# Performance work log

Measured on AMD Instinct MI355X. Metric: run time of the kernel, lower is better.

The kernel has to match this reference:

```python
import jax, jax.numpy as jnp
import numpy as np

B, S, D, H = 2, 2048, 1024, 16
HD = D // H  # head_dim = 64
ROPE_BASE = 10000.0


def setup_inputs() -> dict:
    key = jax.random.key(0)
    ks = jax.random.split(key, 5)
    scale = 1.0 / np.sqrt(D)
    return {
        "x": jax.random.normal(ks[0], (B, S, D), dtype=jnp.float32),
        "Wq": jax.random.normal(ks[1], (D, D), dtype=jnp.float32) * scale,
        "Wk": jax.random.normal(ks[2], (D, D), dtype=jnp.float32) * scale,
        "Wv": jax.random.normal(ks[3], (D, D), dtype=jnp.float32) * scale,
        "Wo": jax.random.normal(ks[4], (D, D), dtype=jnp.float32) * scale,
    }


def _rotate_half(x):
    x1, x2 = x[..., : HD // 2], x[..., HD // 2:]
    return jnp.concatenate((-x2, x1), axis=-1)


def _rope_cos_sin(seq_len):
    inv_freq = 1.0 / (ROPE_BASE ** (jnp.arange(0, HD, 2, dtype=jnp.float32) / HD))
    t = jnp.arange(seq_len, dtype=jnp.float32)
    freqs = jnp.outer(t, inv_freq)          # [S, HD/2]
    emb = jnp.concatenate((freqs, freqs), -1)  # [S, HD]
    return jnp.cos(emb), jnp.sin(emb)


def reference(x, Wq, Wk, Wv, Wo):
    # projections (torch Linear: y = x @ W.T), split heads -> [B, H, S, HD]
    def proj(W):
        return (x @ W.T).reshape(B, S, H, HD).transpose(0, 2, 1, 3)

    q, k, v = proj(Wq), proj(Wk), proj(Wv)

    cos, sin = _rope_cos_sin(S)  # [S, HD] each, broadcast over B, H
    q = q * cos + _rotate_half(q) * sin
    k = k * cos + _rotate_half(k) * sin

    scale = 1.0 / np.sqrt(HD)
    scores = jnp.einsum("bhsd,bhtd->bhst", q, k) * scale  # [B,H,S,S]
    attn = jax.nn.softmax(scores, axis=-1)
    out = jnp.einsum("bhst,bhtd->bhsd", attn, v)           # [B,H,S,HD]
    out = out.transpose(0, 2, 1, 3).reshape(B, S, D)
    return out @ Wo.T
```

## Files before the change

### kernel.cpp

```cpp
#include <hip/hip_runtime.h>
#include <hip/hip_bf16.h>
#include <math.h>
#include <stdint.h>

typedef __bf16 bf16;
typedef __bf16 bf16x8 __attribute__((ext_vector_type(8)));
typedef __bf16 bf16x4 __attribute__((ext_vector_type(4)));
typedef float  f32x4  __attribute__((ext_vector_type(4)));

#define MFMA16(a,b,c) __builtin_amdgcn_mfma_f32_16x16x32_bf16((a),(b),(c),0,0,0)
#define GLOAD_LDS16(g, l) \
  __builtin_amdgcn_global_load_lds((__attribute__((address_space(1))) void*)(g), \
                                   (__attribute__((address_space(3))) void*)(l), 16, 0, 0)

static constexpr int kB  = 2;
static constexpr int kS  = 2048;
static constexpr int kD  = 1024;
static constexpr int kH  = 16;
static constexpr int kHD = 64;
static constexpr int kM  = kB * kS;
static constexpr float kExpC = 0.125f * 1.44269504f;

__global__ void cvt_all(const float* __restrict__ x,
                        const float* __restrict__ wq, const float* __restrict__ wk,
                        const float* __restrict__ wv, const float* __restrict__ wo,
                        bf16* __restrict__ xb,
                        bf16* __restrict__ wqb, bf16* __restrict__ wkb,
                        bf16* __restrict__ wvb, bf16* __restrict__ wob,
                        float2* __restrict__ rtab)
{
  const int i = blockIdx.x * 256 + threadIdx.x;
  const int NX4 = (kM * kD) / 4;
  const int NW4 = (kD * kD) / 4;
  if (i >= NX4 + 4 * NW4) {
    const int idx = i - (NX4 + 4 * NW4);
    const int s = idx >> 5, d = idx & 31;
    const float f = exp2f(-(float)d * 0.4152410118609203f);
    float sn, cs;
    sincosf((float)s * f, &sn, &cs);
    rtab[idx] = make_float2(cs, sn);
    return;
  }
  const float* src; bf16* dst; int off;
  if (i < NX4) { src = x; dst = xb; off = i; }
  else {
    const int j = i - NX4;
    const int seg = j >> 18;
    off = j & (NW4 - 1);
    src = (seg == 0) ? wq : (seg == 1) ? wk : (seg == 2) ? wv : wo;
    dst = (seg == 0) ? wqb : (seg == 1) ? wkb : (seg == 2) ? wvb : wob;
  }
  const float4 v = ((const float4*)src)[off];
  bf16x4 o = { (bf16)v.x, (bf16)v.y, (bf16)v.z, (bf16)v.w };
  ((bf16x4*)dst)[off] = o;
}

__device__ __forceinline__ void gemm_core_128(
    const bf16* __restrict__ A, const bf16* __restrict__ Bw,
    int m0, int n0, int K, bf16* aT, bf16* bT, f32x4 acc[4][4])
{
  const int t = threadIdx.x, lane = t & 63, wave = t >> 6;
  const int wm = wave >> 1, wn = wave & 1;
  const int srow = lane >> 2;
  const int scol = (lane & 3) * 8;
  for (int k0 = 0; k0 < K; k0 += 32) {
    __syncthreads();
#pragma unroll
    for (int c = 0; c < 2; ++c) {
      const int row = c * 64 + wave * 16 + srow;
      const bf16* ga = A  + (size_t)(m0 + row) * K + k0 + scol;
      const bf16* gb = Bw + (size_t)(n0 + row) * K + k0 + scol;
      GLOAD_LDS16(ga, aT + c * 2048 + wave * 512);
      GLOAD_LDS16(gb, bT + c * 2048 + wave * 512);
    }
    __syncthreads();
    bf16x8 af[4], bfr[4];
#pragma unroll
    for (int i = 0; i < 4; ++i) {
      af[i]  = *(const bf16x8*)(aT + (wm * 64 + i * 16 + (lane & 15)) * 32 + (lane >> 4) * 8);
      bfr[i] = *(const bf16x8*)(bT + (wn * 64 + i * 16 + (lane & 15)) * 32 + (lane >> 4) * 8);
    }
#pragma unroll
    for (int i = 0; i < 4; ++i)
#pragma unroll
      for (int j = 0; j < 4; ++j)
        acc[i][j] = MFMA16(af[i], bfr[j], acc[i][j]);
  }
}

__global__ __launch_bounds__(256) void proj_qkv(
    const bf16* __restrict__ xb,
    const bf16* __restrict__ wqb, const bf16* __restrict__ wkb, const bf16* __restrict__ wvb,
    bf16* __restrict__ Qb, bf16* __restrict__ Kb, bf16* __restrict__ Vt,
    const float2* __restrict__ rtab)
{
  __shared__ __align__(16) bf16 aT[4096];
  __shared__ __align__(16) bf16 bT[4096];
  __shared__ __align__(16) bf16 vtr[2 * 64 * 136];
  const int z = blockIdx.z;
  const bf16* Ww = (z == 0) ? wqb : (z == 1) ? wkb : wvb;
  const int m0 = blockIdx.x * 128, n0 = blockIdx.y * 128;
  f32x4 acc[4][4] = {};
  gemm_core_128(xb, Ww, m0, n0, kD, aT, bT, acc);

  const int lane = threadIdx.x & 63, wave = threadIdx.x >> 6;
  const int wm = wave >> 1, wn = wave & 1, quad = lane >> 4, lc = lane & 15;
  const int hh = (n0 >> 6) + wn;
  if (z == 2) {
#pragma unroll
    for (int i = 0; i < 4; ++i)
#pragma unroll
      for (int j = 0; j < 4; ++j) {
        bf16x4 p;
#pragma unroll
        for (int r = 0; r < 4; ++r) p[r] = (bf16)acc[i][j][r];
        *(bf16x4*)&vtr[(wn * 64 + j * 16 + lc) * 136 + wm * 64 + i * 16 + quad * 4] = p;
      }
    __syncthreads();
    const int t = threadIdx.x;
    const int row = t >> 1;
    const int sh = (t & 1) * 64;
    const int bidx = m0 >> 11;
    const int hh2 = (n0 >> 6) + (row >> 6);
    const int d = row & 63;
    bf16* dst = Vt + ((size_t)(bidx * kH + hh2) * kHD + d) * kS + (m0 & 2047) + sh;
#pragma unroll
    for (int u = 0; u < 8; ++u)
      *(uint4*)(dst + u * 8) = *(const uint4*)&vtr[row * 136 + sh + u * 8];
  } else {
    bf16* Op = (z == 0) ? Qb : Kb;
    const float f = (z == 0) ? kExpC : 1.0f;
#pragma unroll
    for (int j = 0; j < 2; ++j) {
      const int d = j * 16 + lc;
#pragma unroll
      for (int i = 0; i < 4; ++i)
#pragma unroll
        for (int r = 0; r < 4; ++r) {
          const int m = m0 + wm * 64 + i * 16 + quad * 4 + r;
          const int bidx = m >> 11, s = m & 2047;
          const float2 cs = rtab[s * 32 + d];
          const float v0 = acc[i][j][r], v1 = acc[i][j + 2][r];
          bf16* dst = Op + ((size_t)(bidx * kH + hh) * kS + s) * kHD;
          dst[d]      = (bf16)((v0 * cs.x - v1 * cs.y) * f);
          dst[d + 32] = (bf16)((v1 * cs.x + v0 * cs.y) * f);
        }
    }
  }
}

__global__ __launch_bounds__(256, 2) void attn(
    const bf16* __restrict__ Qb, const bf16* __restrict__ Kb,
    const bf16* __restrict__ Vt, bf16* __restrict__ Ob)
{
  __shared__ __align__(16) bf16 kT[128 * 72];
  __shared__ __align__(16) bf16 vT[64 * 136];
  const int t = threadIdx.x, lane = t & 63, wave = t >> 6;
  const int quad = lane >> 4, lc = lane & 15;
  const int bid = blockIdx.x;
  const int qt = (bid >> 3) & 15;
  const int bh = (bid & 7) * 4 + (bid >> 7);
  const size_t base = (size_t)bh * kS * kHD;
  const bf16* Qp = Qb + base + (size_t)qt * 128 * kHD;
  const bf16* Kp = Kb + base;
  const bf16* Vp = Vt + base;

  bf16x8 qf[2][2];
#pragma unroll
  for (int tm = 0; tm < 2; ++tm)
#pragma unroll
    for (int ks = 0; ks < 2; ++ks)
      qf[tm][ks] = *(const bf16x8*)(Qp + (wave * 32 + tm * 16 + lc) * kHD + ks * 32 + quad * 8);

  f32x4 oacc[2][4] = {};
  f32x4 lacc[2] = {};
  const bf16 one = (bf16)1.0f;
  const bf16x8 ones = { one, one, one, one, one, one, one, one };

  const int srow = t >> 1, shalf = (t & 1) * 32;
  const int vd = t >> 2, vc = t & 3;

  for (int kt = 0; kt < kS / 128; ++kt) {
    __syncthreads();
    {
      const bf16* ksrc = Kp + (size_t)(kt * 128 + srow) * kHD + shalf;
#pragma unroll
      for (int u = 0; u < 4; ++u)
        *(uint4*)&kT[srow * 72 + shalf + u * 8] = *(const uint4*)(ksrc + u * 8);
      const bf16* vsrc = Vp + (size_t)vd * kS + kt * 128 + vc * 32;
#pragma unroll
      for (int u = 0; u < 4; ++u)
        *(uint4*)&vT[vd * 136 + vc * 32 + u * 8] = *(const uint4*)(vsrc + u * 8);
    }
    __syncthreads();

    bf16x8 kf[8][2];
#pragma unroll
    for (int nk = 0; nk < 8; ++nk)
#pragma unroll
      for (int ks = 0; ks < 2; ++ks)
        kf[nk][ks] = *(const bf16x8*)&kT[(nk * 16 + lc) * 72 + ks * 32 + quad * 8];

    bf16x8 pfrag[2][4];
#pragma unroll
    for (int tm = 0; tm < 2; ++tm) {
      f32x4 sc[8] = {};
#pragma unroll
      for (int nk = 0; nk < 8; ++nk) {
        sc[nk] = MFMA16(kf[nk][0], qf[tm][0], sc[nk]);
        sc[nk] = MFMA16(kf[nk][1], qf[tm][1], sc[nk]);
      }
#pragma unroll
      for (int kp = 0; kp < 4; ++kp) {
        bf16x8 p;
#pragma unroll
        for (int j = 0; j < 4; ++j) {
          p[j]     = (bf16)__builtin_amdgcn_exp2f(sc[2 * kp][j]);
          p[j + 4] = (bf16)__builtin_amdgcn_exp2f(sc[2 * kp + 1][j]);
        }
        pfrag[tm][kp] = p;
      }
    }

#pragma unroll
    for (int kp = 0; kp < 4; ++kp)
#pragma unroll
      for (int tm = 0; tm < 2; ++tm)
        lacc[tm] = MFMA16(pfrag[tm][kp], ones, lacc[tm]);

#pragma unroll
    for (int nd = 0; nd < 4; ++nd)
#pragma unroll
      for (int kp = 0; kp < 4; ++kp) {
        const bf16x4 lo = *(const bf16x4*)&vT[(nd * 16 + lc) * 136 + kp * 32 + quad * 4];
        const bf16x4 hi = *(const bf16x4*)&vT[(nd * 16 + lc) * 136 + kp * 32 + 16 + quad * 4];
        const bf16x8 vfr = __builtin_shufflevector(lo, hi, 0, 1, 2, 3, 4, 5, 6, 7);
#pragma unroll
        for (int tm = 0; tm < 2; ++tm)
          oacc[tm][nd] = MFMA16(pfrag[tm][kp], vfr, oacc[tm][nd]);
      }
  }

  const int b = bh >> 4, h = bh & 15;
#pragma unroll
  for (int tm = 0; tm < 2; ++tm)
#pragma unroll
    for (int r = 0; r < 4; ++r) {
      const float inv = 1.0f / lacc[tm][r];
      const int s = qt * 128 + wave * 32 + tm * 16 + quad * 4 + r;
      bf16* dst = Ob + ((size_t)(b * kS + s)) * kD + h * kHD;
#pragma unroll
      for (int nd = 0; nd < 4; ++nd)
        dst[nd * 16 + lc] = (bf16)(oacc[tm][nd][r] * inv);
    }
}

__global__ __launch_bounds__(256) void out_proj(
    const bf16* __restrict__ Ab, const bf16* __restrict__ wob, float* __restrict__ Cout)
{
  __shared__ __align__(16) bf16 aT[4096];
  __shared__ __align__(16) bf16 bT[4096];
  const int m0 = blockIdx.x * 128, n0 = blockIdx.y * 128;
  f32x4 acc[4][4] = {};
  gemm_core_128(Ab, wob, m0, n0, kD, aT, bT, acc);
  const int lane = threadIdx.x & 63, wave = threadIdx.x >> 6;
  const int wm = wave >> 1, wn = wave & 1, quad = lane >> 4, lc = lane & 15;
#pragma unroll
  for (int i = 0; i < 4; ++i)
#pragma unroll
    for (int r = 0; r < 4; ++r) {
      const int m = m0 + wm * 64 + i * 16 + quad * 4 + r;
#pragma unroll
      for (int j = 0; j < 4; ++j)
        Cout[(size_t)m * kD + n0 + wn * 64 + j * 16 + lc] = acc[i][j][r];
    }
}

extern "C" void kernel_launch(void* const* d_in, const int* in_sizes, int n_in,
                              void* d_out, int out_size, void* d_ws, size_t ws_size,
                              hipStream_t stream)
{
  const float* x  = (const float*)d_in[0];
  const float* wq = (const float*)d_in[1];
  const float* wk = (const float*)d_in[2];
  const float* wv = (const float*)d_in[3];
  const float* wo = (const float*)d_in[4];
  float* out = (float*)d_out;

  char* ws = (char*)d_ws;
  const size_t MB = 1024 * 1024;
  if (ws_size < 57 * MB) return;
  bf16* xb  = (bf16*)(ws + 0 * MB);
  bf16* wqb = (bf16*)(ws + 8 * MB);
  bf16* wkb = (bf16*)(ws + 10 * MB);
  bf16* wvb = (bf16*)(ws + 12 * MB);
  bf16* wob = (bf16*)(ws + 14 * MB);
  bf16* Qb  = (bf16*)(ws + 16 * MB);
  bf16* Kb  = (bf16*)(ws + 24 * MB);
  bf16* Ob  = (bf16*)(ws + 40 * MB);
  float2* rtab = (float2*)(ws + 48 * MB);
  bf16* Vtp = (bf16*)(ws + 49 * MB);

  cvt_all<<<8448, 256, 0, stream>>>(x, wq, wk, wv, wo, xb, wqb, wkb, wvb, wob, rtab);
  proj_qkv<<<dim3(32, 8, 3), 256, 0, stream>>>(xb, wqb, wkb, wvb, Qb, Kb, Vtp, rtab);
  attn<<<dim3(512), 256, 0, stream>>>(Qb, Kb, Vtp, Ob);
  out_proj<<<dim3(32, 8), 256, 0, stream>>>(Ob, wob, out);
}
```

Baseline: 194.0 us.

## Register-prefetch next tiles in GEMM and attention loops to overlap loads

Both the shared GEMM core and the attention kernel now load the next K-step or KV tile from global memory into registers before computing on the current tile. That data is written to LDS at the start of the next iteration. The GEMM drops the direct global-to-LDS load path in favour of a register-staged double buffer. The aim is to hide global memory latency behind the MFMA work, at the cost of more registers, a possible occupancy drop, and one redundant wraparound load on the last iteration.

Result: slower. 231.3 us (+19.2%).

```diff
diff --git a/kernel.cpp b/kernel.cpp
--- a/kernel.cpp
+++ b/kernel.cpp
@@ -9,9 +9,6 @@
 typedef float  f32x4  __attribute__((ext_vector_type(4)));
 
 #define MFMA16(a,b,c) __builtin_amdgcn_mfma_f32_16x16x32_bf16((a),(b),(c),0,0,0)
-#define GLOAD_LDS16(g, l) \
-  __builtin_amdgcn_global_load_lds((__attribute__((address_space(1))) void*)(g), \
-                                   (__attribute__((address_space(3))) void*)(l), 16, 0, 0)
 
 static constexpr int kB  = 2;
 static constexpr int kS  = 2048;
@@ -63,16 +60,27 @@
   const int wm = wave >> 1, wn = wave & 1;
   const int srow = lane >> 2;
   const int scol = (lane & 3) * 8;
+  const bf16* ga0 = A  + (size_t)(m0 + wave * 16 + srow) * K + scol;
+  const bf16* ga1 = ga0 + (size_t)64 * K;
+  const bf16* gb0 = Bw + (size_t)(n0 + wave * 16 + srow) * K + scol;
+  const bf16* gb1 = gb0 + (size_t)64 * K;
+  bf16* const wa0 = aT + wave * 512 + lane * 8;
+  bf16* const wb0 = bT + wave * 512 + lane * 8;
+
+  bf16x8 ra0 = *(const bf16x8*)ga0;
+  bf16x8 ra1 = *(const bf16x8*)ga1;
+  bf16x8 rb0 = *(const bf16x8*)gb0;
+  bf16x8 rb1 = *(const bf16x8*)gb1;
+
   for (int k0 = 0; k0 < K; k0 += 32) {
-    __syncthreads();
-#pragma unroll
-    for (int c = 0; c < 2; ++c) {
-      const int row = c * 64 + wave * 16 + srow;
-      const bf16* ga = A  + (size_t)(m0 + row) * K + k0 + scol;
-      const bf16* gb = Bw + (size_t)(n0 + row) * K + k0 + scol;
-      GLOAD_LDS16(ga, aT + c * 2048 + wave * 512);
-      GLOAD_LDS16(gb, bT + c * 2048 + wave * 512);
-    }
+    const int kn = (k0 + 32 < K) ? (k0 + 32) : 0;
+    const bf16x8 na0 = *(const bf16x8*)(ga0 + kn);
+    const bf16x8 na1 = *(const bf16x8*)(ga1 + kn);
+    const bf16x8 nb0 = *(const bf16x8*)(gb0 + kn);
+    const bf16x8 nb1 = *(const bf16x8*)(gb1 + kn);
+    __syncthreads();
+    *(bf16x8*)wa0 = ra0;  *(bf16x8*)(wa0 + 2048) = ra1;
+    *(bf16x8*)wb0 = rb0;  *(bf16x8*)(wb0 + 2048) = rb1;
     __syncthreads();
     bf16x8 af[4], bfr[4];
 #pragma unroll
@@ -85,6 +93,7 @@
 #pragma unroll
       for (int j = 0; j < 4; ++j)
         acc[i][j] = MFMA16(af[i], bfr[j], acc[i][j]);
+    ra0 = na0; ra1 = na1; rb0 = nb0; rb1 = nb1;
   }
 }
 
@@ -180,19 +189,36 @@
   const int srow = t >> 1, shalf = (t & 1) * 32;
   const int vd = t >> 2, vc = t & 3;
 
+  uint4 rk[4], rv[4];
+  {
+    const bf16* ksrc = Kp + (size_t)srow * kHD + shalf;
+    const bf16* vsrc = Vp + (size_t)vd * kS + vc * 32;
+#pragma unroll
+    for (int u = 0; u < 4; ++u) rk[u] = ((const uint4*)ksrc)[u];
+#pragma unroll
+    for (int u = 0; u < 4; ++u) rv[u] = ((const uint4*)vsrc)[u];
+  }
+
   for (int kt = 0; kt < kS / 128; ++kt) {
     __syncthreads();
+#pragma unroll
+    for (int u = 0; u < 4; ++u)
+      *(uint4*)&kT[srow * 72 + shalf + u * 8] = rk[u];
+#pragma unroll
+    for (int u = 0; u < 4; ++u)
+      *(uint4*)&vT[vd * 136 + vc * 32 + u * 8] = rv[u];
+    __syncthreads();
+
+    const int ktn = (kt + 1 < kS / 128) ? kt + 1 : 0;
+    uint4 nk_[4], nv_[4];
     {
-      const bf16* ksrc = Kp + (size_t)(kt * 128 + srow) * kHD + shalf;
-#pragma unroll
-      for (int u = 0; u < 4; ++u)
-        *(uint4*)&kT[srow * 72 + shalf + u * 8] = *(const uint4*)(ksrc + u * 8);
-      const bf16* vsrc = Vp + (size_t)vd * kS + kt * 128 + vc * 32;
-#pragma unroll
-      for (int u = 0; u < 4; ++u)
-        *(uint4*)&vT[vd * 136 + vc * 32 + u * 8] = *(const uint4*)(vsrc + u * 8);
-    }
-    __syncthreads();
+      const bf16* ksrc = Kp + (size_t)(ktn * 128 + srow) * kHD + shalf;
+      const bf16* vsrc = Vp + (size_t)vd * kS + ktn * 128 + vc * 32;
+#pragma unroll
+      for (int u = 0; u < 4; ++u) nk_[u] = ((const uint4*)ksrc)[u];
+#pragma unroll
+      for (int u = 0; u < 4; ++u) nv_[u] = ((const uint4*)vsrc)[u];
+    }
 
     bf16x8 kf[8][2];
 #pragma unroll
@@ -239,6 +265,9 @@
         for (int tm = 0; tm < 2; ++tm)
           oacc[tm][nd] = MFMA16(pfrag[tm][kp], vfr, oacc[tm][nd]);
       }
+
+#pragma unroll
+    for (int u = 0; u < 4; ++u) { rk[u] = nk_[u]; rv[u] = nv_[u]; }
   }
 
   const int b = bh >> 4, h = bh & 15;
```
